# Kernel optimization log

Hardware: AMD Instinct MI355X
Metric: run time of the kernel (lower is better)

## Reference

```python
import jax, jax.numpy as jnp
import numpy as np

B, S, H, A = 32, 2048, 1024, 1024  # batch, seq, enc_hid_dim, arg_dim


def setup_inputs() -> dict:
    key = jax.random.key(0)
    k1, k2, k3, k4, k5, k6, k7, k8 = jax.random.split(key, 8)
    arg1 = jax.random.normal(k1, (B, A), dtype=jnp.float32)
    arg2 = jax.random.normal(k2, (B, A), dtype=jnp.float32)
    enc_hs = jax.random.normal(k3, (B, S, H), dtype=jnp.float32)
    src_mask = jax.random.randint(k4, (B, S), 0, 2).astype(bool)  # True = masked
    # nn.Linear(H+A, 1): weight [1, H+A], bias [1]; store as vector + scalar
    bound = 1.0 / np.sqrt(H + A)
    w1_w = jax.random.uniform(k5, (H + A,), jnp.float32, -bound, bound)
    w1_b = jax.random.uniform(k6, (), jnp.float32, -bound, bound)
    w2_w = jax.random.uniform(k7, (H + A,), jnp.float32, -bound, bound)
    w2_b = jax.random.uniform(k8, (), jnp.float32, -bound, bound)
    return {"arg1": arg1, "arg2": arg2, "enc_hs": enc_hs, "src_mask": src_mask,
            "w1_w": w1_w, "w1_b": w1_b, "w2_w": w2_w, "w2_b": w2_b}


def _attend(enc_hs, arg, w, b, src_mask):
    # Equivalent to Linear(cat(enc_hs, arg_broadcast)) without materializing concat:
    # score[b,s] = enc_hs[b,s] . w[:H] + arg[b] . w[H:] + b
    s_enc = jnp.einsum('bsh,h->bs', enc_hs, w[:H])          # [B,S]
    s_arg = jnp.einsum('ba,a->b', arg, w[H:])               # [B]
    score = s_enc + s_arg[:, None] + b                      # [B,S]
    score = jnp.where(src_mask, -jnp.inf, score)
    att = jax.nn.softmax(score, axis=-1)                    # [B,S]
    return jnp.einsum('bs,bsh->bh', att, enc_hs)            # [B,H]


def reference(arg1, arg2, enc_hs, src_mask, w1_w, w1_b, w2_w, w2_b):
    ctx1 = _attend(enc_hs, arg1, w1_w, w1_b, src_mask)
    ctx2 = _attend(enc_hs, arg2, w2_w, w2_b, src_mask)
    return jnp.concatenate((ctx1, ctx2), axis=-1)           # [B, 2H]
```

## Files before the change

kernel.cpp:

```cpp
#include <hip/hip_runtime.h>

#define BB 32
#define SS 2048
#define HH 1024
#define NCHUNK 32
#define ROWS_PER_CHUNK 64
#define ROWS_PER_WAVE 16

__device__ __forceinline__ float dot4(float4 a, float4 b) {
    return a.x * b.x + a.y * b.y + a.z * b.z + a.w * b.w;
}
__device__ __forceinline__ void fma4(float4& a, float p, float4 r) {
    a.x += p * r.x; a.y += p * r.y; a.z += p * r.z; a.w += p * r.w;
}
__device__ __forceinline__ void add4(float4& a, float4 r) {
    a.x += r.x; a.y += r.y; a.z += r.z; a.w += r.w;
}

__global__ __launch_bounds__(256, 4) void attn_partial(
    const float* __restrict__ enc,
    const int* __restrict__ mask,
    const float* __restrict__ w1,
    const float* __restrict__ w2,
    float* __restrict__ pnum,
    float* __restrict__ pl)
{
    const int tid  = threadIdx.x;
    const int wave = tid >> 6;
    const int lane = tid & 63;
    const int b     = blockIdx.x / NCHUNK;
    const int chunk = blockIdx.x % NCHUNK;
    const int s0 = chunk * ROWS_PER_CHUNK + wave * ROWS_PER_WAVE;

    const float4* w1v = (const float4*)w1;
    const float4* w2v = (const float4*)w2;
    float4 wa0 = w1v[lane], wa1 = w1v[lane + 64], wa2 = w1v[lane + 128], wa3 = w1v[lane + 192];
    float4 wb0 = w2v[lane], wb1 = w2v[lane + 64], wb2 = w2v[lane + 128], wb3 = w2v[lane + 192];

    float4 z = {0.f, 0.f, 0.f, 0.f};
    float4 a0 = z, a1 = z, a2 = z, a3 = z;
    float4 c0 = z, c1 = z, c2 = z, c3 = z;
    float l1 = 0.f, l2 = 0.f;

    const int*    mrow = mask + (size_t)b * SS;
    const float4* encb = (const float4*)(enc + (size_t)b * SS * HH);

    for (int i = 0; i < ROWS_PER_WAVE; ++i) {
        const int s = s0 + i;
        if (mrow[s]) continue;
        const float4* row = encb + (size_t)s * (HH / 4);
        float4 r0 = row[lane];
        float4 r1 = row[lane + 64];
        float4 r2 = row[lane + 128];
        float4 r3 = row[lane + 192];
        float d1 = dot4(r0, wa0) + dot4(r1, wa1) + dot4(r2, wa2) + dot4(r3, wa3);
        float d2 = dot4(r0, wb0) + dot4(r1, wb1) + dot4(r2, wb2) + dot4(r3, wb3);
#pragma unroll
        for (int off = 32; off; off >>= 1) {
            d1 += __shfl_xor(d1, off, 64);
            d2 += __shfl_xor(d2, off, 64);
        }
        const float p1 = __expf(d1);
        const float p2 = __expf(d2);
        l1 += p1; l2 += p2;
        fma4(a0, p1, r0); fma4(a1, p1, r1); fma4(a2, p1, r2); fma4(a3, p1, r3);
        fma4(c0, p2, r0); fma4(c1, p2, r1); fma4(c2, p2, r2); fma4(c3, p2, r3);
    }

    __shared__ float4 lds[4][2][HH / 4];
    __shared__ float  ldsl[4][2];
    lds[wave][0][lane]       = a0;
    lds[wave][0][lane + 64]  = a1;
    lds[wave][0][lane + 128] = a2;
    lds[wave][0][lane + 192] = a3;
    lds[wave][1][lane]       = c0;
    lds[wave][1][lane + 64]  = c1;
    lds[wave][1][lane + 128] = c2;
    lds[wave][1][lane + 192] = c3;
    if (lane == 0) { ldsl[wave][0] = l1; ldsl[wave][1] = l2; }
    __syncthreads();

    float4 s1 = lds[0][0][tid];
    add4(s1, lds[1][0][tid]); add4(s1, lds[2][0][tid]); add4(s1, lds[3][0][tid]);
    float4 s2 = lds[0][1][tid];
    add4(s2, lds[1][1][tid]); add4(s2, lds[2][1][tid]); add4(s2, lds[3][1][tid]);

    const size_t base = (size_t)(b * NCHUNK + chunk) * 2 * (HH / 4);
    float4* pv = (float4*)pnum;
    pv[base + tid]            = s1;
    pv[base + (HH / 4) + tid] = s2;
    if (tid < 2)
        pl[(b * NCHUNK + chunk) * 2 + tid] =
            ldsl[0][tid] + ldsl[1][tid] + ldsl[2][tid] + ldsl[3][tid];
}

__global__ __launch_bounds__(256) void attn_combine(
    const float* __restrict__ pnum, const float* __restrict__ pl,
    float* __restrict__ out)
{
    const int b = blockIdx.x >> 1;
    const int j = blockIdx.x & 1;
    const int t = threadIdx.x;
    const float4* pv = (const float4*)pnum;
    float4 sum = {0.f, 0.f, 0.f, 0.f};
    float L = 0.f;
    for (int c = 0; c < NCHUNK; ++c) {
        const size_t base = (size_t)((b * NCHUNK + c) * 2 + j) * (HH / 4);
        add4(sum, pv[base + t]);
        L += pl[(b * NCHUNK + c) * 2 + j];
    }
    const float inv = 1.0f / L;
    float4 o = {sum.x * inv, sum.y * inv, sum.z * inv, sum.w * inv};
    ((float4*)out)[((size_t)b * 2 + j) * (HH / 4) + t] = o;
}

extern "C" void kernel_launch(void* const* d_in, const int* in_sizes, int n_in,
                              void* d_out, int out_size, void* d_ws, size_t ws_size,
                              hipStream_t stream) {
    const float* enc  = (const float*)d_in[2];
    const int*   mask = (const int*)d_in[3];
    const float* w1   = (const float*)d_in[4];
    const float* w2   = (const float*)d_in[6];
    float* out  = (float*)d_out;
    float* pnum = (float*)d_ws;
    float* pl   = pnum + (size_t)BB * NCHUNK * 2 * HH;

    attn_partial<<<BB * NCHUNK, 256, 0, stream>>>(enc, mask, w1, w2, pnum, pl);
    attn_combine<<<BB * 2, 256, 0, stream>>>(pnum, pl, out);
}
```

Baseline: 349.3 us.

## Fuse combine into partial kernel via last-block atomic counter, halve chunk count

Removes the separate combine kernel. Each block publishes its partial numerators and sums, bumps a per-batch atomic counter, and the last block for a batch reduces all chunks and writes the output. The chunk count drops from 32 to 16 per batch, which doubles the rows per wave and halves the partial traffic. This saves one kernel launch and partial reloads, but adds a memset, threadfences, and a serialized tail reduction per batch, and leaves only 512 blocks.

```diff
diff --git a/kernel.cpp b/kernel.cpp
--- a/kernel.cpp
+++ b/kernel.cpp
@@ -3,9 +3,9 @@
 #define BB 32
 #define SS 2048
 #define HH 1024
-#define NCHUNK 32
-#define ROWS_PER_CHUNK 64
-#define ROWS_PER_WAVE 16
+#define NCHUNK 16
+#define ROWS_PER_CHUNK 128
+#define ROWS_PER_WAVE 32
 
 __device__ __forceinline__ float dot4(float4 a, float4 b) {
     return a.x * b.x + a.y * b.y + a.z * b.z + a.w * b.w;
@@ -17,13 +17,15 @@
     a.x += r.x; a.y += r.y; a.z += r.z; a.w += r.w;
 }
 
-__global__ __launch_bounds__(256, 4) void attn_partial(
+__global__ __launch_bounds__(256, 4) void attn_fused(
     const float* __restrict__ enc,
     const int* __restrict__ mask,
     const float* __restrict__ w1,
     const float* __restrict__ w2,
     float* __restrict__ pnum,
-    float* __restrict__ pl)
+    float* __restrict__ pl,
+    int* __restrict__ cnt,
+    float* __restrict__ out)
 {
     const int tid  = threadIdx.x;
     const int wave = tid >> 6;
@@ -37,7 +39,7 @@
     float4 wa0 = w1v[lane], wa1 = w1v[lane + 64], wa2 = w1v[lane + 128], wa3 = w1v[lane + 192];
     float4 wb0 = w2v[lane], wb1 = w2v[lane + 64], wb2 = w2v[lane + 128], wb3 = w2v[lane + 192];
 
-    float4 z = {0.f, 0.f, 0.f, 0.f};
+    const float4 z = {0.f, 0.f, 0.f, 0.f};
     float4 a0 = z, a1 = z, a2 = z, a3 = z;
     float4 c0 = z, c1 = z, c2 = z, c3 = z;
     float l1 = 0.f, l2 = 0.f;
@@ -85,33 +87,36 @@
     float4 s2 = lds[0][1][tid];
     add4(s2, lds[1][1][tid]); add4(s2, lds[2][1][tid]); add4(s2, lds[3][1][tid]);
 
+    float4* pv = (float4*)pnum;
     const size_t base = (size_t)(b * NCHUNK + chunk) * 2 * (HH / 4);
-    float4* pv = (float4*)pnum;
     pv[base + tid]            = s1;
     pv[base + (HH / 4) + tid] = s2;
     if (tid < 2)
         pl[(b * NCHUNK + chunk) * 2 + tid] =
             ldsl[0][tid] + ldsl[1][tid] + ldsl[2][tid] + ldsl[3][tid];
-}
 
-__global__ __launch_bounds__(256) void attn_combine(
-    const float* __restrict__ pnum, const float* __restrict__ pl,
-    float* __restrict__ out)
-{
-    const int b = blockIdx.x >> 1;
-    const int j = blockIdx.x & 1;
-    const int t = threadIdx.x;
-    const float4* pv = (const float4*)pnum;
-    float4 sum = {0.f, 0.f, 0.f, 0.f};
-    float L = 0.f;
+    __threadfence();
+    __shared__ int amLast;
+    if (tid == 0) amLast = (atomicAdd(&cnt[b], 1) == NCHUNK - 1);
+    __syncthreads();
+    if (!amLast) return;
+    __threadfence();
+
+    float4 acc1 = z, acc2 = z;
+    float L1 = 0.f, L2 = 0.f;
     for (int c = 0; c < NCHUNK; ++c) {
-        const size_t base = (size_t)((b * NCHUNK + c) * 2 + j) * (HH / 4);
-        add4(sum, pv[base + t]);
-        L += pl[(b * NCHUNK + c) * 2 + j];
+        const size_t pb = (size_t)(b * NCHUNK + c) * 2 * (HH / 4);
+        add4(acc1, pv[pb + tid]);
+        add4(acc2, pv[pb + (HH / 4) + tid]);
+        L1 += pl[(b * NCHUNK + c) * 2 + 0];
+        L2 += pl[(b * NCHUNK + c) * 2 + 1];
     }
-    const float inv = 1.0f / L;
-    float4 o = {sum.x * inv, sum.y * inv, sum.z * inv, sum.w * inv};
-    ((float4*)out)[((size_t)b * 2 + j) * (HH / 4) + t] = o;
+    const float i1 = 1.0f / L1, i2 = 1.0f / L2;
+    float4 o1 = {acc1.x * i1, acc1.y * i1, acc1.z * i1, acc1.w * i1};
+    float4 o2 = {acc2.x * i2, acc2.y * i2, acc2.z * i2, acc2.w * i2};
+    float4* ov = (float4*)out;
+    ov[(size_t)b * 2 * (HH / 4) + tid]            = o1;
+    ov[(size_t)b * 2 * (HH / 4) + (HH / 4) + tid] = o2;
 }
 
 extern "C" void kernel_launch(void* const* d_in, const int* in_sizes, int n_in,
@@ -121,10 +126,12 @@
     const int*   mask = (const int*)d_in[3];
     const float* w1   = (const float*)d_in[4];
     const float* w2   = (const float*)d_in[6];
-    float* out  = (float*)d_out;
-    float* pnum = (float*)d_ws;
+    float* out = (float*)d_out;
+
+    int*   cnt  = (int*)d_ws;
+    float* pnum = (float*)((char*)d_ws + 256);
     float* pl   = pnum + (size_t)BB * NCHUNK * 2 * HH;
 
-    attn_partial<<<BB * NCHUNK, 256, 0, stream>>>(enc, mask, w1, w2, pnum, pl);
-    attn_combine<<<BB * 2, 256, 0, stream>>>(pnum, pl, out);
+    hipMemsetAsync(cnt, 0, BB * sizeof(int), stream);
+    attn_fused<<<BB * NCHUNK, 256, 0, stream>>>(enc, mask, w1, w2, pnum, pl, cnt, out);
 }
```

Result: slower. 425.7 us (+21.9%).
